# Performance work log

Hardware: AMD Instinct MI355X
Metric: run time of the kernel (lower is better)

The kernel has to match this reference:

```python
import jax, jax.numpy as jnp
import numpy as np

BATCH, L, IN_DIM, HID, STATE, MLP, OUT, NUM_LAYERS = 16, 2048, 64, 256, 256, 1024, 128, 4
MAX_PHASE = 2.0 * np.pi


def setup_inputs() -> dict:
    key = jax.random.key(0)
    ks = iter(jax.random.split(key, 32))
    x = jax.random.normal(next(ks), (BATCH, L, IN_DIM), dtype=jnp.float32)
    # embedding Linear(IN_DIM -> HID)
    emb_W = jax.random.normal(next(ks), (HID, IN_DIM), dtype=jnp.float32) / np.sqrt(IN_DIM)
    emb_b = jnp.zeros((HID,), dtype=jnp.float32)
    # LRU params per layer (r_min=0, r_max=1, max_phase=2pi)
    u1 = jax.random.uniform(next(ks), (NUM_LAYERS, STATE), minval=1e-4, maxval=1.0)
    u2 = jax.random.uniform(next(ks), (NUM_LAYERS, STATE), minval=1e-4, maxval=1.0)
    nu_log = jnp.log(-0.5 * jnp.log(u1))
    theta_log = jnp.log(MAX_PHASE * u2)
    lam_abs = jnp.exp(-jnp.exp(nu_log))
    gamma_log = jnp.log(jnp.sqrt(1.0 - lam_abs ** 2))
    B_re = jax.random.normal(next(ks), (NUM_LAYERS, STATE, HID)) / np.sqrt(2 * HID)
    B_im = jax.random.normal(next(ks), (NUM_LAYERS, STATE, HID)) / np.sqrt(2 * HID)
    C_re = jax.random.normal(next(ks), (NUM_LAYERS, HID, STATE)) / np.sqrt(STATE)
    C_im = jax.random.normal(next(ks), (NUM_LAYERS, HID, STATE)) / np.sqrt(STATE)
    D = jax.random.normal(next(ks), (NUM_LAYERS, HID))
    # block MLP: Linear(STATE->MLP), GELU, Linear(MLP->HID)
    Wh = jax.random.normal(next(ks), (NUM_LAYERS, MLP, STATE)) / np.sqrt(STATE)
    bh = jnp.zeros((NUM_LAYERS, MLP), dtype=jnp.float32)
    Wo = jax.random.normal(next(ks), (NUM_LAYERS, HID, MLP)) / np.sqrt(MLP)
    bo = jnp.zeros((NUM_LAYERS, HID), dtype=jnp.float32)
    # output Linear(HID -> OUT)
    out_W = jax.random.normal(next(ks), (OUT, HID), dtype=jnp.float32) / np.sqrt(HID)
    out_b = jnp.zeros((OUT,), dtype=jnp.float32)
    return {"x": x, "emb_W": emb_W, "emb_b": emb_b, "nu_log": nu_log,
            "theta_log": theta_log, "gamma_log": gamma_log, "B_re": B_re,
            "B_im": B_im, "C_re": C_re, "C_im": C_im, "D": D,
            "Wh": Wh, "bh": bh, "Wo": Wo, "bo": bo,
            "out_W": out_W, "out_b": out_b}


def _binop(ei, ej):
    a_i, bu_i = ei
    a_j, bu_j = ej
    return a_j * a_i, a_j * bu_i + bu_j


def _lru(x, nu, th, gl, Bre, Bim, Cre, Cim, D):
    # x: (B, L, H) real; state diag recurrence in complex64
    lam = jnp.exp(-jnp.exp(nu) + 1j * jnp.exp(th))               # (S,)
    B_norm = (Bre + 1j * Bim) * jnp.exp(gl)[:, None]             # (S, H)
    Bu = jnp.einsum("blh,sh->bls", x.astype(B_norm.dtype), B_norm)  # (B, L, S)
    Lam = jnp.broadcast_to(lam, Bu.shape)
    _, states = jax.lax.associative_scan(_binop, (Lam, Bu), axis=1)
    C = Cre + 1j * Cim                                           # (H, S)
    y = jnp.einsum("bls,hs->blh", states, C).real + D * x        # (B, L, H)
    return y


def reference(x, emb_W, emb_b, nu_log, theta_log, gamma_log, B_re, B_im,
              C_re, C_im, D, Wh, bh, Wo, bo, out_W, out_b):
    h = x @ emb_W.T + emb_b                                      # (B, L, HID)
    for l in range(NUM_LAYERS):
        y = _lru(h, nu_log[l], theta_log[l], gamma_log[l],
                 B_re[l], B_im[l], C_re[l], C_im[l], D[l])
        z = jax.nn.gelu(y @ Wh[l].T + bh[l], approximate=False)  # exact GELU as torch
        h = z @ Wo[l].T + bo[l] + y                              # residual
    return h @ out_W.T + out_b                                   # (B, L, OUT)
```

## Files before the change

kernel.cpp:

```cpp
#include <hip/hip_runtime.h>
#include <hip/hip_bf16.h>
#include <math.h>

typedef __hip_bfloat16 bf16;
typedef __attribute__((ext_vector_type(8))) short bf16x8;
typedef __attribute__((ext_vector_type(4))) float f32x4;

#define BATCH   16
#define SEQLEN  2048
#define INDIM   64
#define HIDD    256
#define STATE_D 256
#define MLPD    1024
#define OUTD    128
#define NLAYERS 4
#define M_TOK   (BATCH*SEQLEN)
#define CHUNK   64
#define NCHUNK  (SEQLEN/CHUNK)

__device__ float g_carry[512*512];
__device__ bf16  g_hb [(size_t)M_TOK*256];
__device__ bf16  g_yb [(size_t)M_TOK*256];
__device__ bf16  g_bub[(size_t)M_TOK*512];
__device__ bf16  g_zb [(size_t)M_TOK*1024];
__device__ bf16  g_Bnb[NLAYERS*512*256];
__device__ bf16  g_Cwb[NLAYERS*256*512];
__device__ bf16  g_Whb[NLAYERS*1024*256];
__device__ bf16  g_Wob[NLAYERS*256*1024];

#define SB_HB  0
#define SB_YB  1
#define SB_BUB 2
#define SB_ZB  3
#define SB_BNB 4
#define SB_CWB 5
#define SB_WHB 6
#define SB_WOB 7

__device__ __forceinline__ bf16* bufb(int sel){
  switch(sel){
    case SB_HB:  return g_hb;  case SB_YB:  return g_yb;
    case SB_BUB: return g_bub; case SB_ZB:  return g_zb;
    case SB_BNB: return g_Bnb; case SB_CWB: return g_Cwb;
    case SB_WHB: return g_Whb; default:     return g_Wob; }
}

__device__ __forceinline__ void gld_lds16(const void* g, void* l){
  __builtin_amdgcn_global_load_lds(
      (const __attribute__((address_space(1))) unsigned int*)g,
      (__attribute__((address_space(3))) unsigned int*)l, 16, 0, 0);
}

__device__ __forceinline__ float fast_gelu(float v){
  const float x  = v * 0.70710678118654752f;
  const float ax = fabsf(x);
  const float t  = __builtin_amdgcn_rcpf(fmaf(0.3275911f, ax, 1.0f));
  float p = fmaf(t, 1.061405429f, -1.453152027f);
  p = fmaf(t, p, 1.421413741f);
  p = fmaf(t, p, -0.284496736f);
  p = fmaf(t, p, 0.254829592f);
  p = p * t;
  const float e = __expf(-ax * ax);
  const float erf_ax = fmaf(-p, e, 1.0f);
  const float erf_x  = copysignf(erf_ax, x);
  return 0.5f * v * (1.0f + erf_x);
}

__device__ __forceinline__ void lam_of(const float* __restrict__ nu_log,
                                       const float* __restrict__ th_log,
                                       int s, float& lr, float& li)
{
  float nu  = expf(nu_log[s]);
  float th  = expf(th_log[s]);
  float mag = expf(-nu);
  lr = mag * cosf(th);
  li = mag * sinf(th);
}

#define RPSTR 136

template<int ACT, int FLAGS>
__global__ __launch_bounds__(256, 6) void mfma_gemm(
    int aSel, int lda, int wSel, int wOff, int ldw,
    int oSel, int ldc,
    const float* __restrict__ bias,
    int rSel, int ldres,
    const float* __restrict__ dscale,
    int K,
    const float* __restrict__ nu_log,
    const float* __restrict__ th_log)
{
  const bf16* A = bufb(aSel);
  const bf16* W = bufb(wSel) + wOff;
  bf16* OB = bufb(oSel);
  const bf16* res = (rSel >= 0) ? bufb(rSel) : nullptr;

  __shared__ __align__(16) unsigned short lds[12288];
  unsigned short* As = lds;
  unsigned short* Ws = lds + 4096;

  const int gx = gridDim.x;
  const int nwg = gx * gridDim.y;
  const int orig = blockIdx.y * gx + blockIdx.x;
  const int q = nwg >> 3, r = nwg & 7;
  const int xcd = orig & 7, idx = orig >> 3;
  const int wg = (xcd < r ? xcd*(q+1) : r*(q+1) + (xcd-r)*q) + idx;
  const int bx = wg % gx, by = wg / gx;

  const int tid  = threadIdx.x;
  const int row0 = by * 64, col0 = bx * 128;
  const int lane = tid & 63;
  const int m16  = lane & 15, quad = lane >> 4;
  const int wv   = tid >> 6;
  const int wm   = (wv & 1) * 32, wn = (wv >> 1) * 64;

  const int rlo = wv*16 + (lane >> 2);
  const int sg  = ((lane & 3) ^ ((rlo >> 1) & 3)) * 8;
  const bf16* ga = &A[(size_t)(row0 + rlo)*lda + sg];
  const bf16* gw = &W[(size_t)(col0 + rlo)*ldw + sg];
  const size_t w64 = (size_t)64 * ldw;

  auto STAGE = [&](int bb, int k0){
    unsigned short* Ab = As + bb*2048;
    unsigned short* Wb = Ws + bb*4096;
    gld_lds16(ga + k0,       Ab + wv*512);
    gld_lds16(gw + k0,       Wb + wv*512);
    gld_lds16(gw + k0 + w64, Wb + 2048 + wv*512);
  };

  f32x4 acc[2][4] = {};
  const int nt = K >> 5;

  STAGE(0, 0); STAGE(1, 32);

  for (int t = 0; t < nt; ++t){
    const int b = t & 1;
    if (t + 1 < nt) asm volatile("s_waitcnt vmcnt(3)" ::: "memory");
    else            asm volatile("s_waitcnt vmcnt(0)" ::: "memory");
    __builtin_amdgcn_s_barrier();

    const unsigned short* Ab = As + b*2048;
    const unsigned short* Wb = Ws + b*4096;
    bf16x8 af[2], wf[4];
    #pragma unroll
    for (int i = 0; i < 2; i++){
      const int rA = wm + 16*i + m16;
      af[i] = *reinterpret_cast<const bf16x8*>(&Ab[rA*32 + ((quad ^ ((rA>>1)&3))<<3)]);
    }
    #pragma unroll
    for (int j = 0; j < 4; j++){
      const int rW = wn + 16*j + m16;
      wf[j] = *reinterpret_cast<const bf16x8*>(&Wb[rW*32 + ((quad ^ ((rW>>1)&3))<<3)]);
    }
    asm volatile("s_waitcnt lgkmcnt(0)" ::: "memory");
    __builtin_amdgcn_sched_barrier(0);
    __builtin_amdgcn_s_barrier();

    if (t + 2 < nt) STAGE(b, (t + 2) << 5);

    __builtin_amdgcn_s_setprio(1);
    #pragma unroll
    for (int i = 0; i < 2; i++)
      #pragma unroll
      for (int j = 0; j < 4; j++)
        acc[i][j] = __builtin_amdgcn_mfma_f32_16x16x32_bf16(af[i], wf[j], acc[i][j], 0, 0, 0);
    __builtin_amdgcn_s_setprio(0);
  }

  #pragma unroll
  for (int i = 0; i < 2; i++){
    #pragma unroll
    for (int j = 0; j < 4; j++){
      const int lcol = wn + 16*j + m16;
      const int col  = col0 + lcol;
      #pragma unroll
      for (int r2 = 0; r2 < 4; r2++){
        const int lrow = wm + 16*i + quad*4 + r2;
        const int row  = row0 + lrow;
        float v = acc[i][j][r2];
        if (FLAGS & 1) v += bias[col];
        if (ACT == 1)  v = fast_gelu(v);
        if (FLAGS & 2) v += __bfloat162float(res[(size_t)row*ldres + col]);
        if (FLAGS & 4) v += dscale[col] * __bfloat162float(res[(size_t)row*ldres + col]);
        bf16 bv = __float2bfloat16(v);
        lds[lrow*RPSTR + lcol] = *reinterpret_cast<unsigned short*>(&bv);
      }
    }
  }
  __syncthreads();

  {
    const int rr  = tid >> 4;
    const int c16 = (tid & 15) * 8;
    #pragma unroll
    for (int s = 0; s < 4; s++){
      const int orow = s*16 + rr;
      uint4 d = *reinterpret_cast<const uint4*>(&lds[orow*RPSTR + c16]);
      *reinterpret_cast<uint4*>(OB + (size_t)(row0 + orow)*ldc + col0 + c16) = d;
    }
  }

  if (FLAGS & 8){
    if (tid < 64){
      const int sglob = (col0 >> 1) + tid;
      float lr, li; lam_of(nu_log, th_log, sglob, lr, li);
      float ar = 0.f, ai = 0.f;
      for (int t = 0; t < CHUNK; t++){
        unsigned int pr = *reinterpret_cast<const unsigned int*>(&lds[t*RPSTR + 2*tid]);
        float br = __uint_as_float(pr << 16);
        float bi = __uint_as_float(pr & 0xffff0000u);
        float nr = fmaf(lr, ar, fmaf(-li, ai, br));
        float ni = fmaf(lr, ai, fmaf( li, ar, bi));
        ar = nr; ai = ni;
      }
      g_carry[(size_t)by*512 + 2*sglob]     = ar;
      g_carry[(size_t)by*512 + 2*sglob + 1] = ai;
    }
  }
}

__global__ __launch_bounds__(256) void emb_gemm(
    const float* __restrict__ x, const float* __restrict__ W,
    const float* __restrict__ b)
{
  __shared__ __align__(16) float Asx[16][68];
  __shared__ __align__(16) float Wsx[16][68];
  const int tid = threadIdx.x;
  const int tx = tid & 15, ty = tid >> 4;
  const int row0 = blockIdx.y * 64, col0 = blockIdx.x * 64;
  const int lc = tid & 15, lr = tid >> 4;
  float acc[4][4] = {};
  for (int k0 = 0; k0 < INDIM; k0 += 16){
    #pragma unroll
    for (int i = 0; i < 4; i++){
      Asx[lc][lr + 16*i] = x[(size_t)(row0 + lr + 16*i)*INDIM + k0 + lc];
      Wsx[lc][lr + 16*i] = W[(size_t)(col0 + lr + 16*i)*INDIM + k0 + lc];
    }
    __syncthreads();
    #pragma unroll
    for (int k = 0; k < 16; k++){
      float4 av = *reinterpret_cast<const float4*>(&Asx[k][ty*4]);
      float4 bv = *reinterpret_cast<const float4*>(&Wsx[k][tx*4]);
      float a[4] = {av.x, av.y, av.z, av.w};
      float b2[4] = {bv.x, bv.y, bv.z, bv.w};
      #pragma unroll
      for (int i = 0; i < 4; i++)
        #pragma unroll
        for (int j = 0; j < 4; j++)
          acc[i][j] = fmaf(a[i], b2[j], acc[i][j]);
    }
    __syncthreads();
  }
  #pragma unroll
  for (int i = 0; i < 4; i++){
    const int r = row0 + ty*4 + i;
    #pragma unroll
    for (int j = 0; j < 4; j++){
      const int cn = col0 + tx*4 + j;
      g_hb[(size_t)r*HIDD + cn] = __float2bfloat16(acc[i][j] + b[cn]);
    }
  }
}

__global__ __launch_bounds__(256) void out_gemm(
    const float* __restrict__ W, const float* __restrict__ b,
    float* __restrict__ out)
{
  __shared__ __align__(16) float Asx[16][68];
  __shared__ __align__(16) float Wsx[16][68];
  const int tid = threadIdx.x;
  const int tx = tid & 15, ty = tid >> 4;
  const int row0 = blockIdx.y * 64, col0 = blockIdx.x * 64;
  const int lc = tid & 15, lr = tid >> 4;
  float acc[4][4] = {};
  for (int k0 = 0; k0 < HIDD; k0 += 16){
    #pragma unroll
    for (int i = 0; i < 4; i++){
      Asx[lc][lr + 16*i] = __bfloat162float(g_hb[(size_t)(row0 + lr + 16*i)*HIDD + k0 + lc]);
      Wsx[lc][lr + 16*i] = W[(size_t)(col0 + lr + 16*i)*HIDD + k0 + lc];
    }
    __syncthreads();
    #pragma unroll
    for (int k = 0; k < 16; k++){
      float4 av = *reinterpret_cast<const float4*>(&Asx[k][ty*4]);
      float4 bv = *reinterpret_cast<const float4*>(&Wsx[k][tx*4]);
      float a[4] = {av.x, av.y, av.z, av.w};
      float b2[4] = {bv.x, bv.y, bv.z, bv.w};
      #pragma unroll
      for (int i = 0; i < 4; i++)
        #pragma unroll
        for (int j = 0; j < 4; j++)
          acc[i][j] = fmaf(a[i], b2[j], acc[i][j]);
    }
    __syncthreads();
  }
  #pragma unroll
  for (int i = 0; i < 4; i++){
    const int r = row0 + ty*4 + i;
    #pragma unroll
    for (int j = 0; j < 4; j++){
      const int cn = col0 + tx*4 + j;
      out[(size_t)r*OUTD + cn] = acc[i][j] + b[cn];
    }
  }
}

__global__ __launch_bounds__(256) void scan_fix(
    const float* __restrict__ nu_log, const float* __restrict__ th_log)
{
  const int blk = blockIdx.x;
  const int c   = blk & (NCHUNK - 1);
  const int s   = threadIdx.x;
  float lr, li; lam_of(nu_log, th_log, s, lr, li);
  float cr = 0.f, ci = 0.f;
  if (c > 0){
    float Tr = lr, Ti = li;
    #pragma unroll
    for (int i = 0; i < 6; i++){ float nr = Tr*Tr - Ti*Ti; Ti = 2.f*Tr*Ti; Tr = nr; }
    const int bstart = blk - c;
    for (int j = 0; j < c; j++){
      float2 e = *reinterpret_cast<const float2*>(&g_carry[(size_t)(bstart + j)*512 + 2*s]);
      float nr = fmaf(Tr, cr, fmaf(-Ti, ci, e.x));
      float ni = fmaf(Tr, ci, fmaf( Ti, cr, e.y));
      cr = nr; ci = ni;
    }
  }
  float ar = cr, ai = ci;
  unsigned int* pb = reinterpret_cast<unsigned int*>(g_bub) + (size_t)blk*CHUNK*256 + s;
  for (int t = 0; t < CHUNK; t++){
    unsigned int pr = pb[(size_t)t*256];
    float br = __uint_as_float(pr << 16);
    float bi = __uint_as_float(pr & 0xffff0000u);
    float nr = fmaf(lr, ar, fmaf(-li, ai, br));
    float ni = fmaf(lr, ai, fmaf( li, ar, bi));
    ar = nr; ai = ni;
    bf16 hr = __float2bfloat16(ar), hi2 = __float2bfloat16(ai);
    unsigned int w = (unsigned int)(*reinterpret_cast<unsigned short*>(&hr))
                   | ((unsigned int)(*reinterpret_cast<unsigned short*>(&hi2)) << 16);
    pb[(size_t)t*256] = w;
  }
}

__global__ __launch_bounds__(256) void pack_B(
    const float* __restrict__ Bre, const float* __restrict__ Bim,
    const float* __restrict__ gl)
{
  int idx = blockIdx.x * 256 + threadIdx.x;
  int l = idx >> 16, within = idx & 65535;
  int s = within >> 8, h = within & 255;
  float g = expf(gl[l*STATE_D + s]);
  g_Bnb[(size_t)l*131072 + (size_t)(2*s  )*256 + h] = __float2bfloat16(Bre[idx] * g);
  g_Bnb[(size_t)l*131072 + (size_t)(2*s+1)*256 + h] = __float2bfloat16(Bim[idx] * g);
}

__global__ __launch_bounds__(256) void pack_C(
    const float* __restrict__ Cre, const float* __restrict__ Cim)
{
  int idx = blockIdx.x * 256 + threadIdx.x;
  int l = idx >> 16, within = idx & 65535;
  int h = within >> 8, s = within & 255;
  g_Cwb[(size_t)l*131072 + (size_t)h*512 + 2*s]     = __float2bfloat16( Cre[idx]);
  g_Cwb[(size_t)l*131072 + (size_t)h*512 + 2*s + 1] = __float2bfloat16(-Cim[idx]);
}

__global__ __launch_bounds__(256) void conv_bf16(
    const float* __restrict__ src, int dstSel, int n)
{
  int i = blockIdx.x * 256 + threadIdx.x;
  if (i < n) bufb(dstSel)[i] = __float2bfloat16(src[i]);
}

extern "C" void kernel_launch(void* const* d_in, const int* in_sizes, int n_in,
                              void* d_out, int out_size, void* d_ws, size_t ws_size,
                              hipStream_t stream)
{
  (void)d_ws; (void)ws_size; (void)out_size; (void)n_in; (void)in_sizes;
  const float* x      = (const float*)d_in[0];
  const float* emb_W  = (const float*)d_in[1];
  const float* emb_b  = (const float*)d_in[2];
  const float* nu_log = (const float*)d_in[3];
  const float* th_log = (const float*)d_in[4];
  const float* ga_log = (const float*)d_in[5];
  const float* B_re   = (const float*)d_in[6];
  const float* B_im   = (const float*)d_in[7];
  const float* C_re   = (const float*)d_in[8];
  const float* C_im   = (const float*)d_in[9];
  const float* Dv     = (const float*)d_in[10];
  const float* Wh     = (const float*)d_in[11];
  const float* bh     = (const float*)d_in[12];
  const float* Wo     = (const float*)d_in[13];
  const float* bo     = (const float*)d_in[14];
  const float* out_W  = (const float*)d_in[15];
  const float* out_b  = (const float*)d_in[16];

  const dim3 blk(256);

  pack_B<<<dim3(NLAYERS*256), blk, 0, stream>>>(B_re, B_im, ga_log);
  pack_C<<<dim3(NLAYERS*256), blk, 0, stream>>>(C_re, C_im);
  conv_bf16<<<dim3(NLAYERS*1024), blk, 0, stream>>>(Wh, SB_WHB, NLAYERS*262144);
  conv_bf16<<<dim3(NLAYERS*1024), blk, 0, stream>>>(Wo, SB_WOB, NLAYERS*262144);

  emb_gemm<<<dim3(HIDD/64, M_TOK/64), blk, 0, stream>>>(x, emb_W, emb_b);

  for (int l = 0; l < NLAYERS; l++){
    mfma_gemm<0, 8><<<dim3(4, M_TOK/64), blk, 0, stream>>>(
        SB_HB, HIDD, SB_BNB, l*131072, HIDD, SB_BUB, 512,
        nullptr, -1, 0, nullptr, HIDD,
        nu_log + l*STATE_D, th_log + l*STATE_D);

    scan_fix<<<dim3(M_TOK/CHUNK), blk, 0, stream>>>(nu_log + l*STATE_D, th_log + l*STATE_D);

    mfma_gemm<0, 4><<<dim3(2, M_TOK/64), blk, 0, stream>>>(
        SB_BUB, 512, SB_CWB, l*131072, 512, SB_YB, HIDD,
        nullptr, SB_HB, HIDD, Dv + l*HIDD, 512, nullptr, nullptr);

    mfma_gemm<1, 1><<<dim3(8, M_TOK/64), blk, 0, stream>>>(
        SB_YB, HIDD, SB_WHB, l*262144, STATE_D, SB_ZB, MLPD,
        bh + l*MLPD, -1, 0, nullptr, STATE_D, nullptr, nullptr);

    mfma_gemm<0, 3><<<dim3(2, M_TOK/64), blk, 0, stream>>>(
        SB_ZB, MLPD, SB_WOB, l*262144, MLPD, SB_HB, HIDD,
        bo + l*HIDD, SB_YB, HIDD, nullptr, MLPD, nullptr, nullptr);
  }

  out_gemm<<<dim3(OUTD/64, M_TOK/64), blk, 0, stream>>>(out_W, out_b, (float*)d_out);
}
```

Baseline: 809.9 us.

## Fuse MLP up-projection, GELU and down-projection into one kernel

Result: faster. 751.7 us (-7.2%).

```diff
diff --git a/kernel.cpp b/kernel.cpp
--- a/kernel.cpp
+++ b/kernel.cpp
@@ -22,7 +22,6 @@
 __device__ bf16  g_hb [(size_t)M_TOK*256];
 __device__ bf16  g_yb [(size_t)M_TOK*256];
 __device__ bf16  g_bub[(size_t)M_TOK*512];
-__device__ bf16  g_zb [(size_t)M_TOK*1024];
 __device__ bf16  g_Bnb[NLAYERS*512*256];
 __device__ bf16  g_Cwb[NLAYERS*256*512];
 __device__ bf16  g_Whb[NLAYERS*1024*256];
@@ -31,7 +30,6 @@
 #define SB_HB  0
 #define SB_YB  1
 #define SB_BUB 2
-#define SB_ZB  3
 #define SB_BNB 4
 #define SB_CWB 5
 #define SB_WHB 6
@@ -40,7 +38,7 @@
 __device__ __forceinline__ bf16* bufb(int sel){
   switch(sel){
     case SB_HB:  return g_hb;  case SB_YB:  return g_yb;
-    case SB_BUB: return g_bub; case SB_ZB:  return g_zb;
+    case SB_BUB: return g_bub;
     case SB_BNB: return g_Bnb; case SB_CWB: return g_Cwb;
     case SB_WHB: return g_Whb; default:     return g_Wob; }
 }
@@ -66,6 +64,15 @@
   return 0.5f * v * (1.0f + erf_x);
 }
 
+__device__ __forceinline__ unsigned int bf2_add(unsigned int a, unsigned int b){
+  float alo = __uint_as_float(a << 16), ahi = __uint_as_float(a & 0xffff0000u);
+  float blo = __uint_as_float(b << 16), bhi = __uint_as_float(b & 0xffff0000u);
+  bf16 l = __float2bfloat16(alo + blo);
+  bf16 h = __float2bfloat16(ahi + bhi);
+  return (unsigned int)(*reinterpret_cast<unsigned short*>(&l))
+       | ((unsigned int)(*reinterpret_cast<unsigned short*>(&h)) << 16);
+}
+
 __device__ __forceinline__ void lam_of(const float* __restrict__ nu_log,
                                        const float* __restrict__ th_log,
                                        int s, float& lr, float& li)
@@ -215,6 +222,167 @@
       }
       g_carry[(size_t)by*512 + 2*sglob]     = ar;
       g_carry[(size_t)by*512 + 2*sglob + 1] = ai;
+    }
+  }
+}
+
+__global__ __launch_bounds__(256, 2) void fused_mlp(
+    int whOff, int woOff,
+    const float* __restrict__ bh, const float* __restrict__ bo)
+{
+  const bf16* Wh = g_Whb + whOff;
+  const bf16* Wo = g_Wob + woOff;
+
+  __shared__ __align__(16) unsigned short As[2*2048];
+  __shared__ __align__(16) unsigned short Ws[2*8192];
+  __shared__ __align__(16) unsigned short zbuf[64*132];
+
+  const int tid  = threadIdx.x;
+  const int row0 = blockIdx.x * 64;
+  const int lane = tid & 63;
+  const int m16  = lane & 15, quad = lane >> 4;
+  const int wv   = tid >> 6;
+  const int wm   = (wv & 1) * 32;
+  const int wnA  = (wv >> 1) * 64;
+  const int wnB  = (wv >> 1) * 128;
+
+  const int rlo = wv*16 + (lane >> 2);
+  const int sg  = ((lane & 3) ^ ((rlo >> 1) & 3)) * 8;
+
+  const bf16* ga = g_yb + (size_t)(row0 + rlo)*HIDD + sg;
+
+  f32x4 accB[2][8] = {};
+
+  for (int mc = 0; mc < 8; ++mc){
+    const bf16* gwh = Wh + (size_t)(mc*128 + rlo)*HIDD + sg;
+    const bf16* gwo = Wo + (size_t)rlo*MLPD + mc*128 + sg;
+
+    auto STAGE_A = [&](int b, int k0){
+      gld_lds16(ga + k0,            As + b*2048 + wv*512);
+      gld_lds16(gwh + k0,           Ws + b*8192 + wv*512);
+      gld_lds16(gwh + k0 + 64*HIDD, Ws + b*8192 + 2048 + wv*512);
+    };
+    auto STAGE_B = [&](int b, int ks){
+      const bf16* src = gwo + ks*32;
+      #pragma unroll
+      for (int g = 0; g < 4; g++)
+        gld_lds16(src + (size_t)g*64*MLPD, Ws + b*8192 + g*2048 + wv*512);
+    };
+
+    f32x4 accA[2][4] = {};
+    STAGE_A(0, 0); STAGE_A(1, 32);
+    for (int t = 0; t < 8; ++t){
+      const int b = t & 1;
+      if (t + 1 < 8) asm volatile("s_waitcnt vmcnt(3)" ::: "memory");
+      else           asm volatile("s_waitcnt vmcnt(0)" ::: "memory");
+      __builtin_amdgcn_s_barrier();
+      const unsigned short* Ab = As + b*2048;
+      const unsigned short* Wb = Ws + b*8192;
+      bf16x8 af[2], wf[4];
+      #pragma unroll
+      for (int i = 0; i < 2; i++){
+        const int rA = wm + 16*i + m16;
+        af[i] = *reinterpret_cast<const bf16x8*>(&Ab[rA*32 + ((quad ^ ((rA>>1)&3))<<3)]);
+      }
+      #pragma unroll
+      for (int j = 0; j < 4; j++){
+        const int rW = wnA + 16*j + m16;
+        wf[j] = *reinterpret_cast<const bf16x8*>(&Wb[rW*32 + ((quad ^ ((rW>>1)&3))<<3)]);
+      }
+      asm volatile("s_waitcnt lgkmcnt(0)" ::: "memory");
+      __builtin_amdgcn_sched_barrier(0);
+      __builtin_amdgcn_s_barrier();
+      if (t + 2 < 8) STAGE_A(b, (t + 2) << 5);
+      __builtin_amdgcn_s_setprio(1);
+      #pragma unroll
+      for (int i = 0; i < 2; i++)
+        #pragma unroll
+        for (int j = 0; j < 4; j++)
+          accA[i][j] = __builtin_amdgcn_mfma_f32_16x16x32_bf16(af[i], wf[j], accA[i][j], 0, 0, 0);
+      __builtin_amdgcn_s_setprio(0);
+    }
+    STAGE_B(0, 0); STAGE_B(1, 1);
+
+    #pragma unroll
+    for (int i = 0; i < 2; i++){
+      #pragma unroll
+      for (int j = 0; j < 4; j++){
+        const int lcol = wnA + 16*j + m16;
+        const float bb = bh[mc*128 + lcol];
+        #pragma unroll
+        for (int r2 = 0; r2 < 4; r2++){
+          const int lrow = wm + 16*i + quad*4 + r2;
+          float v = fast_gelu(accA[i][j][r2] + bb);
+          bf16 bv = __float2bfloat16(v);
+          zbuf[lrow*132 + lcol] = *reinterpret_cast<unsigned short*>(&bv);
+        }
+      }
+    }
+    __syncthreads();
+
+    for (int ks = 0; ks < 4; ++ks){
+      const int b = ks & 1;
+      if (ks + 1 < 4) asm volatile("s_waitcnt vmcnt(4)" ::: "memory");
+      else            asm volatile("s_waitcnt vmcnt(0)" ::: "memory");
+      __builtin_amdgcn_s_barrier();
+      const unsigned short* Wb = Ws + b*8192;
+      bf16x8 af[2], wf[8];
+      #pragma unroll
+      for (int i = 0; i < 2; i++){
+        const int rA = wm + 16*i + m16;
+        af[i] = *reinterpret_cast<const bf16x8*>(&zbuf[rA*132 + ks*32 + quad*8]);
+      }
+      #pragma unroll
+      for (int j = 0; j < 8; j++){
+        const int rW = wnB + 16*j + m16;
+        wf[j] = *reinterpret_cast<const bf16x8*>(&Wb[rW*32 + ((quad ^ ((rW>>1)&3))<<3)]);
+      }
+      asm volatile("s_waitcnt lgkmcnt(0)" ::: "memory");
+      __builtin_amdgcn_sched_barrier(0);
+      __builtin_amdgcn_s_barrier();
+      if (ks + 2 < 4) STAGE_B(b, ks + 2);
+      __builtin_amdgcn_s_setprio(1);
+      #pragma unroll
+      for (int i = 0; i < 2; i++)
+        #pragma unroll
+        for (int j = 0; j < 8; j++)
+          accB[i][j] = __builtin_amdgcn_mfma_f32_16x16x32_bf16(af[i], wf[j], accB[i][j], 0, 0, 0);
+      __builtin_amdgcn_s_setprio(0);
+    }
+  }
+
+  #pragma unroll
+  for (int n = 0; n < 2; n++){
+    __syncthreads();
+    if ((wv >> 1) == n){
+      #pragma unroll
+      for (int i = 0; i < 2; i++){
+        #pragma unroll
+        for (int j = 0; j < 8; j++){
+          const int lcol = 16*j + m16;
+          const float bb = bo[n*128 + lcol];
+          #pragma unroll
+          for (int r2 = 0; r2 < 4; r2++){
+            const int lrow = wm + 16*i + quad*4 + r2;
+            float v = accB[i][j][r2] + bb;
+            bf16 bv = __float2bfloat16(v);
+            zbuf[lrow*132 + lcol] = *reinterpret_cast<unsigned short*>(&bv);
+          }
+        }
+      }
+    }
+    __syncthreads();
+    const int rr = tid >> 4, c16 = (tid & 15) * 8;
+    #pragma unroll
+    for (int s = 0; s < 4; s++){
+      const int orow = s*16 + rr;
+      uint4 hv = *reinterpret_cast<const uint4*>(&zbuf[orow*132 + c16]);
+      const size_t go = (size_t)(row0 + orow)*HIDD + n*128 + c16;
+      uint4 yv = *reinterpret_cast<const uint4*>(g_yb + go);
+      uint4 o;
+      o.x = bf2_add(hv.x, yv.x); o.y = bf2_add(hv.y, yv.y);
+      o.z = bf2_add(hv.z, yv.z); o.w = bf2_add(hv.w, yv.w);
+      *reinterpret_cast<uint4*>(g_hb + go) = o;
     }
   }
 }
@@ -414,13 +582,8 @@
         SB_BUB, 512, SB_CWB, l*131072, 512, SB_YB, HIDD,
         nullptr, SB_HB, HIDD, Dv + l*HIDD, 512, nullptr, nullptr);
 
-    mfma_gemm<1, 1><<<dim3(8, M_TOK/64), blk, 0, stream>>>(
-        SB_YB, HIDD, SB_WHB, l*262144, STATE_D, SB_ZB, MLPD,
-        bh + l*MLPD, -1, 0, nullptr, STATE_D, nullptr, nullptr);
-
-    mfma_gemm<0, 3><<<dim3(2, M_TOK/64), blk, 0, stream>>>(
-        SB_ZB, MLPD, SB_WOB, l*262144, MLPD, SB_HB, HIDD,
-        bo + l*HIDD, SB_YB, HIDD, nullptr, MLPD, nullptr, nullptr);
+    fused_mlp<<<dim3(M_TOK/64), blk, 0, stream>>>(
+        l*262144, l*262144, bh + l*MLPD, bo + l*HIDD);
   }
 
   out_gemm<<<dim3(OUTD/64, M_TOK/64), blk, 0, stream>>>(out_W, out_b, (float*)d_out);
```
